# Kernel tuning notes

Measured on AMD Instinct MI355X. Metric: run time of the kernel, lower is better.

## Reference

```python
import jax, jax.numpy as jnp
import numpy as np

ALPHA = 0.2  # LeakyReLU negative slope
NEG_BIG = -9e15


def setup_inputs() -> dict:
    key = jax.random.key(0)
    k1, k2, k3, k4 = jax.random.split(key, 4)
    B, N, Fin, Fout = 16, 1024, 256, 256
    h = jax.random.normal(k1, (B, N, Fin), dtype=jnp.float32)
    adj = jax.random.randint(k2, (B, N, N), 0, 2, dtype=jnp.int32)
    # xavier_uniform with gain=1.414
    def xavier(k, shape, gain=1.414):
        fan_in, fan_out = shape[0], shape[1]
        bound = gain * np.sqrt(6.0 / (fan_in + fan_out))
        return jax.random.uniform(k, shape, jnp.float32, -bound, bound)
    W = xavier(k3, (Fin, Fout))
    a = xavier(k4, (2 * Fout, 1))
    return {"h": h, "adj": adj, "W": W, "a": a}


def reference(h, adj, W, a):
    # h: [B,N,Fin], adj: [B,N,N], W: [Fin,Fout], a: [2*Fout,1]
    Fout = W.shape[1]
    Wh = jnp.einsum('bnf,fo->bno', h, W)                      # [B,N,Fout]
    a1, a2 = a[:Fout, 0], a[Fout:, 0]                          # [Fout], [Fout]
    # e_ij = leakyrelu(Wh_i . a1 + Wh_j . a2) -- outer sum, no O(N^2*F) tensor
    f1 = Wh @ a1                                               # [B,N]
    f2 = Wh @ a2                                               # [B,N]
    e = jax.nn.leaky_relu(f1[:, :, None] + f2[:, None, :], negative_slope=ALPHA)
    attention = jnp.where(adj > 0, e, jnp.float32(NEG_BIG))    # [B,N,N]
    attention = jax.nn.softmax(attention, axis=2)
    h_prime = jnp.einsum('bij,bjo->bio', attention, Wh)        # [B,N,Fout]
    return jax.nn.elu(h_prime)
```

## Files before the change

### kernel.cpp

```cpp
#include <hip/hip_runtime.h>
#include <hip/hip_bf16.h>

#define Bsz 16
#define Nn  1024
#define Ff  256
#define ALPHA 0.2f
#define NEG_BIG -9.0e15f

typedef __attribute__((ext_vector_type(8))) short short8;
typedef __attribute__((ext_vector_type(4))) float f32x4;
typedef __attribute__((ext_vector_type(4))) unsigned short ushort4_t;

__device__ __forceinline__ unsigned short f2bf(float x) {
    union { __hip_bfloat16 b; unsigned short u; } cv;
    cv.b = __float2bfloat16(x);
    return cv.u;
}

__global__ __launch_bounds__(256) void gat_prep(
    const float* __restrict__ W, const float* __restrict__ a,
    float* __restrict__ w1, float* __restrict__ w2)
{
    const int t = threadIdx.x, w = t >> 6, ln = t & 63;
    __shared__ float a1s[Ff], a2s[Ff];
    a1s[t] = a[t];
    a2s[t] = a[Ff + t];
    __syncthreads();
    const int f = blockIdx.x * 4 + w;
    float s1 = 0.f, s2 = 0.f;
    #pragma unroll
    for (int c = 0; c < 4; c++) {
        const int o = ln + 64 * c;
        const float wv = W[(size_t)f * Ff + o];
        s1 += wv * a1s[o];
        s2 += wv * a2s[o];
    }
    #pragma unroll
    for (int off = 1; off < 64; off <<= 1) {
        s1 += __shfl_xor(s1, off, 64);
        s2 += __shfl_xor(s2, off, 64);
    }
    if (ln == 0) { w1[f] = s1; w2[f] = s2; }
}

__global__ __launch_bounds__(256) void pack_f(
    const float* __restrict__ h, const float* __restrict__ W,
    const float* __restrict__ w1, const float* __restrict__ w2,
    unsigned short* __restrict__ hK, unsigned short* __restrict__ WK,
    float* __restrict__ f1, float* __restrict__ f2)
{
    __shared__ __align__(16) float tile[32][258];
    const int id = blockIdx.x, t = threadIdx.x, w = t >> 6, ln = t & 63;
    const bool isH = (id < 512);
    const float* src;
    unsigned short* dst;
    int grow0 = 0;
    if (isH) {
        const int b = id >> 5, kt = id & 31;
        grow0 = b * Nn + kt * 32;
        src = h + (size_t)grow0 * Ff;
        dst = hK + ((size_t)(b * 32 + kt)) * 8192;
    } else {
        const int ft = id - 512;
        src = W + (size_t)ft * 32 * Ff;
        dst = WK + (size_t)ft * 8192;
    }
    #pragma unroll
    for (int rr = 0; rr < 8; rr++) {
        const int row = rr * 4 + w;
        const int col = ln * 4;
        const float4 v = *(const float4*)&src[row * Ff + col];
        float2* tr = (float2*)&tile[row][col];
        tr[0] = make_float2(v.x, v.y);
        tr[1] = make_float2(v.z, v.w);
    }
    __syncthreads();

    unsigned* d32 = (unsigned*)dst;
    #pragma unroll
    for (int k = 0; k < 16; k++) {
        const int fidx = k * 256 + t;
        const int o = fidx >> 4, q = fidx & 15;
        const unsigned lo = f2bf(tile[2 * q][o]);
        const unsigned hi = f2bf(tile[2 * q + 1][o]);
        d32[fidx] = lo | (hi << 16);
    }

    if (isH) {
        float w1r[4], w2r[4];
        #pragma unroll
        for (int c = 0; c < 4; c++) {
            w1r[c] = w1[ln + 64 * c];
            w2r[c] = w2[ln + 64 * c];
        }
        #pragma unroll
        for (int rr = 0; rr < 8; rr++) {
            const int row = rr * 4 + w;
            float s1 = 0.f, s2 = 0.f;
            #pragma unroll
            for (int c = 0; c < 4; c++) {
                const float hv = tile[row][ln + 64 * c];
                s1 += hv * w1r[c];
                s2 += hv * w2r[c];
            }
            #pragma unroll
            for (int off = 1; off < 64; off <<= 1) {
                s1 += __shfl_xor(s1, off, 64);
                s2 += __shfl_xor(s2, off, 64);
            }
            if (ln == 0) { f1[grow0 + row] = s1; f2[grow0 + row] = s2; }
        }
    }
}

#define TI 32
__global__ __launch_bounds__(1024, 8) void gat_attn(
    const int* __restrict__ adj,
    const float* __restrict__ f1, const float* __restrict__ f2,
    const unsigned short* __restrict__ hK, const unsigned short* __restrict__ WK,
    float* __restrict__ out)
{
    __shared__ __align__(16) unsigned short pbf[TI * 1024];
    const int t = threadIdx.x, w = t >> 6, ln = t & 63;
    const int m = ln & 15, quad = ln >> 4;
    const int bid = blockIdx.x;
    const int b  = 2 * (bid & 7) + ((bid >> 3) & 1);
    const int i0 = (bid >> 4) * TI;

    const int r0 = 2 * w, r1 = r0 + 1;
    const int grb = b * Nn + i0 + r0;
    const int* aptr = adj + (size_t)grb * Nn;
    int4 av0[4], av1[4];
    #pragma unroll
    for (int c = 0; c < 4; c++) {
        av0[c] = *(const int4*)&aptr[c * 256 + 4 * ln];
        av1[c] = *(const int4*)&aptr[Nn + c * 256 + 4 * ln];
    }
    float4 f2r[4];
    #pragma unroll
    for (int c = 0; c < 4; c++)
        f2r[c] = *(const float4*)&f2[b * Nn + 256 * c + 4 * ln];

    const float fi0 = f1[grb], fi1 = f1[grb + 1];
    float e0[16], e1[16];
    float mx0 = -INFINITY, mx1 = -INFINITY;
    #pragma unroll
    for (int c = 0; c < 4; c++) {
        const float4 fv = f2r[c];
        float x, y;
        x = fi0 + fv.x; x = fmaxf(x, ALPHA * x); x = av0[c].x > 0 ? x : NEG_BIG; e0[4*c+0] = x;
        y = fi0 + fv.y; y = fmaxf(y, ALPHA * y); y = av0[c].y > 0 ? y : NEG_BIG; e0[4*c+1] = y;
        mx0 = fmaxf(fmaxf(x, y), mx0);
        x = fi0 + fv.z; x = fmaxf(x, ALPHA * x); x = av0[c].z > 0 ? x : NEG_BIG; e0[4*c+2] = x;
        y = fi0 + fv.w; y = fmaxf(y, ALPHA * y); y = av0[c].w > 0 ? y : NEG_BIG; e0[4*c+3] = y;
        mx0 = fmaxf(fmaxf(x, y), mx0);
        x = fi1 + fv.x; x = fmaxf(x, ALPHA * x); x = av1[c].x > 0 ? x : NEG_BIG; e1[4*c+0] = x;
        y = fi1 + fv.y; y = fmaxf(y, ALPHA * y); y = av1[c].y > 0 ? y : NEG_BIG; e1[4*c+1] = y;
        mx1 = fmaxf(fmaxf(x, y), mx1);
        x = fi1 + fv.z; x = fmaxf(x, ALPHA * x); x = av1[c].z > 0 ? x : NEG_BIG; e1[4*c+2] = x;
        y = fi1 + fv.w; y = fmaxf(y, ALPHA * y); y = av1[c].w > 0 ? y : NEG_BIG; e1[4*c+3] = y;
        mx1 = fmaxf(fmaxf(x, y), mx1);
    }
    #pragma unroll
    for (int off = 1; off < 64; off <<= 1) {
        mx0 = fmaxf(mx0, __shfl_xor(mx0, off, 64));
        mx1 = fmaxf(mx1, __shfl_xor(mx1, off, 64));
    }
    float s0 = 0.f, s1 = 0.f;
    #pragma unroll
    for (int c = 0; c < 16; c++) {
        e0[c] = __expf(e0[c] - mx0); s0 += e0[c];
        e1[c] = __expf(e1[c] - mx1); s1 += e1[c];
    }
    #pragma unroll
    for (int off = 1; off < 64; off <<= 1) {
        s0 += __shfl_xor(s0, off, 64);
        s1 += __shfl_xor(s1, off, 64);
    }
    const float ri0 = 1.f / s0, ri1 = 1.f / s1;
    const int sw0 = (r0 & 7) << 3, sw1 = (r1 & 7) << 3;
    #pragma unroll
    for (int c = 0; c < 4; c++) {
        const int j = 256 * c + 4 * ln;
        ushort4_t v0 = { f2bf(e0[4*c] * ri0), f2bf(e0[4*c+1] * ri0),
                         f2bf(e0[4*c+2] * ri0), f2bf(e0[4*c+3] * ri0) };
        ushort4_t v1 = { f2bf(e1[4*c] * ri1), f2bf(e1[4*c+1] * ri1),
                         f2bf(e1[4*c+2] * ri1), f2bf(e1[4*c+3] * ri1) };
        *(ushort4_t*)&pbf[r0 * 1024 + (j ^ sw0)] = v0;
        *(ushort4_t*)&pbf[r1 * 1024 + (j ^ sw1)] = v1;
    }

    const int n0 = w * 16;
    const unsigned short* hKb = hK + (size_t)b * 32 * 8192;
    const int arow0 = m * 1024, arow1 = (16 + m) * 1024;
    const int asw = (m & 7) << 3;
    #define AF0(kt) (*(const short8*)&pbf[arow0 + ((((kt) * 32) + quad * 8) ^ asw)])
    #define AF1(kt) (*(const short8*)&pbf[arow1 + ((((kt) * 32) + quad * 8) ^ asw)])
    #define BF(kt)  (*(const short8*)&hKb[(size_t)(kt) * 8192 + (n0 + m) * 32 + quad * 8])

    short8 bq0 = BF(0), bq1 = BF(1), bq2 = BF(2), bq3 = BF(3);
    __syncthreads();

    f32x4 acc0 = {0.f, 0.f, 0.f, 0.f}, acc1 = acc0;
    short8 a0c = AF0(0), a1c = AF1(0);
    __builtin_amdgcn_s_setprio(1);
    #pragma unroll
    for (int kt = 0; kt < 32; kt++) {
        short8 bnew = bq0, a0n = a0c, a1n = a1c;
        if (kt + 4 < 32) bnew = BF(kt + 4);
        if (kt + 1 < 32) { a0n = AF0(kt + 1); a1n = AF1(kt + 1); }
        acc0 = __builtin_amdgcn_mfma_f32_16x16x32_bf16(a0c, bq0, acc0, 0, 0, 0);
        acc1 = __builtin_amdgcn_mfma_f32_16x16x32_bf16(a1c, bq0, acc1, 0, 0, 0);
        a0c = a0n; a1c = a1n;
        bq0 = bq1; bq1 = bq2; bq2 = bq3; bq3 = bnew;
    }
    __builtin_amdgcn_s_setprio(0);

    #define WB(kt)  (*(const short8*)&WK[(size_t)(kt) * 8192 + (n0 + m) * 32 + quad * 8])
    short8 wbc = WB(0), wbn = WB(1);

    __syncthreads();
    #pragma unroll
    for (int reg = 0; reg < 4; reg++) {
        pbf[(quad * 4 + reg) * 264 + n0 + m]      = f2bf(acc0[reg]);
        pbf[(16 + quad * 4 + reg) * 264 + n0 + m] = f2bf(acc1[reg]);
    }
    __syncthreads();

    #define GA0(kt) (*(const short8*)&pbf[m * 264 + (kt) * 32 + quad * 8])
    #define GA1(kt) (*(const short8*)&pbf[(16 + m) * 264 + (kt) * 32 + quad * 8])

    f32x4 c0 = {0.f, 0.f, 0.f, 0.f}, c1 = c0;
    short8 ga0 = GA0(0), ga1 = GA1(0);
    __builtin_amdgcn_s_setprio(1);
    #pragma unroll
    for (int kt = 0; kt < 8; kt++) {
        short8 ga0n = ga0, ga1n = ga1, wnew = wbc;
        if (kt + 2 < 8) wnew = WB(kt + 2);
        if (kt + 1 < 8) { ga0n = GA0(kt + 1); ga1n = GA1(kt + 1); }
        c0 = __builtin_amdgcn_mfma_f32_16x16x32_bf16(ga0, wbc, c0, 0, 0, 0);
        c1 = __builtin_amdgcn_mfma_f32_16x16x32_bf16(ga1, wbc, c1, 0, 0, 0);
        ga0 = ga0n; ga1 = ga1n; wbc = wbn; wbn = wnew;
    }
    __builtin_amdgcn_s_setprio(0);
    const size_t ob = (size_t)(b * Nn) + i0;
    #pragma unroll
    for (int reg = 0; reg < 4; reg++) {
        float v;
        v = c0[reg]; v = v > 0.f ? v : (__expf(v) - 1.f);
        out[(ob + quad * 4 + reg) * Ff + n0 + m] = v;
        v = c1[reg]; v = v > 0.f ? v : (__expf(v) - 1.f);
        out[(ob + 16 + quad * 4 + reg) * Ff + n0 + m] = v;
    }
}

extern "C" void kernel_launch(void* const* d_in, const int* in_sizes, int n_in,
                              void* d_out, int out_size, void* d_ws, size_t ws_size,
                              hipStream_t stream)
{
    const void* h   = d_in[0];
    const void* adj = d_in[1];
    const void* W   = d_in[2];
    const void* a   = d_in[3];
    for (int i = 0; i < n_in; i++) {
        if      (in_sizes[i] == Bsz * Nn * Ff) h   = d_in[i];
        else if (in_sizes[i] == Bsz * Nn * Nn) adj = d_in[i];
        else if (in_sizes[i] == Ff * Ff)       W   = d_in[i];
        else if (in_sizes[i] == 2 * Ff)        a   = d_in[i];
    }
    float* out = (float*)d_out;

    char*  wsb = (char*)d_ws;
    float* w1  = (float*)wsb;
    float* w2  = w1 + Ff;
    float* f1  = (float*)(wsb + 4096);
    float* f2  = f1 + Bsz * Nn;
    unsigned short* hK = (unsigned short*)(wsb + 4096 + 2 * 65536);
    unsigned short* WK = hK + (size_t)Bsz * 32 * 8192;

    gat_prep<<<64, 256, 0, stream>>>((const float*)W, (const float*)a, w1, w2);
    pack_f<<<520, 256, 0, stream>>>((const float*)h, (const float*)W, w1, w2, hK, WK, f1, f2);
    gat_attn<<<Bsz * (Nn / TI), 1024, 0, stream>>>((const int*)adj, f1, f2, hK, WK, out);
}
```

Before: 138.7 us.

## Precompute Wh=hW in pack kernel and drop second GEMM from attention kernel

Reassociates (P·h)·W into P·(h·W): the pack kernel now multiplies h by W with MFMA and stores bf16 Wh tiles, and the WK bf16 packing moves into the prep kernel. The attention kernel then needs only one GEMM, removing the per-tile W GEMM, its LDS staging and two barriers. It adds an extra bf16 rounding of Wh and more work in the pack stage, and pads the LDS row stride.

```diff
diff --git a/kernel.cpp b/kernel.cpp
--- a/kernel.cpp
+++ b/kernel.cpp
@@ -19,52 +19,35 @@
 
 __global__ __launch_bounds__(256) void gat_prep(
     const float* __restrict__ W, const float* __restrict__ a,
-    float* __restrict__ w1, float* __restrict__ w2)
+    float* __restrict__ w1, float* __restrict__ w2,
+    unsigned short* __restrict__ WK)
 {
     const int t = threadIdx.x, w = t >> 6, ln = t & 63;
-    __shared__ float a1s[Ff], a2s[Ff];
-    a1s[t] = a[t];
-    a2s[t] = a[Ff + t];
-    __syncthreads();
-    const int f = blockIdx.x * 4 + w;
-    float s1 = 0.f, s2 = 0.f;
-    #pragma unroll
-    for (int c = 0; c < 4; c++) {
-        const int o = ln + 64 * c;
-        const float wv = W[(size_t)f * Ff + o];
-        s1 += wv * a1s[o];
-        s2 += wv * a2s[o];
-    }
-    #pragma unroll
-    for (int off = 1; off < 64; off <<= 1) {
-        s1 += __shfl_xor(s1, off, 64);
-        s2 += __shfl_xor(s2, off, 64);
-    }
-    if (ln == 0) { w1[f] = s1; w2[f] = s2; }
-}
-
-__global__ __launch_bounds__(256) void pack_f(
-    const float* __restrict__ h, const float* __restrict__ W,
-    const float* __restrict__ w1, const float* __restrict__ w2,
-    unsigned short* __restrict__ hK, unsigned short* __restrict__ WK,
-    float* __restrict__ f1, float* __restrict__ f2)
-{
+    if (blockIdx.x < 64) {
+        __shared__ float a1s[Ff], a2s[Ff];
+        a1s[t] = a[t];
+        a2s[t] = a[Ff + t];
+        __syncthreads();
+        const int f = blockIdx.x * 4 + w;
+        float s1 = 0.f, s2 = 0.f;
+        #pragma unroll
+        for (int c = 0; c < 4; c++) {
+            const int o = ln + 64 * c;
+            const float wv = W[(size_t)f * Ff + o];
+            s1 += wv * a1s[o];
+            s2 += wv * a2s[o];
+        }
+        #pragma unroll
+        for (int off = 1; off < 64; off <<= 1) {
+            s1 += __shfl_xor(s1, off, 64);
+            s2 += __shfl_xor(s2, off, 64);
+        }
+        if (ln == 0) { w1[f] = s1; w2[f] = s2; }
+        return;
+    }
     __shared__ __align__(16) float tile[32][258];
-    const int id = blockIdx.x, t = threadIdx.x, w = t >> 6, ln = t & 63;
-    const bool isH = (id < 512);
-    const float* src;
-    unsigned short* dst;
-    int grow0 = 0;
-    if (isH) {
-        const int b = id >> 5, kt = id & 31;
-        grow0 = b * Nn + kt * 32;
-        src = h + (size_t)grow0 * Ff;
-        dst = hK + ((size_t)(b * 32 + kt)) * 8192;
-    } else {
-        const int ft = id - 512;
-        src = W + (size_t)ft * 32 * Ff;
-        dst = WK + (size_t)ft * 8192;
-    }
+    const int ft = blockIdx.x - 64;
+    const float* src = W + (size_t)ft * 32 * Ff;
     #pragma unroll
     for (int rr = 0; rr < 8; rr++) {
         const int row = rr * 4 + w;
@@ -75,8 +58,7 @@
         tr[1] = make_float2(v.z, v.w);
     }
     __syncthreads();
-
-    unsigned* d32 = (unsigned*)dst;
+    unsigned* d32 = (unsigned*)(WK + (size_t)ft * 8192);
     #pragma unroll
     for (int k = 0; k < 16; k++) {
         const int fidx = k * 256 + t;
@@ -85,8 +67,30 @@
         const unsigned hi = f2bf(tile[2 * q + 1][o]);
         d32[fidx] = lo | (hi << 16);
     }
-
-    if (isH) {
+}
+
+__global__ __launch_bounds__(256) void pack_f(
+    const float* __restrict__ h, const unsigned short* __restrict__ WK,
+    const float* __restrict__ w1, const float* __restrict__ w2,
+    unsigned short* __restrict__ WhK,
+    float* __restrict__ f1, float* __restrict__ f2)
+{
+    __shared__ __align__(16) float tile[32][258];
+    const int id = blockIdx.x, t = threadIdx.x, w = t >> 6, ln = t & 63;
+    const int grow0 = id * 32;
+    const float* src = h + (size_t)grow0 * Ff;
+    #pragma unroll
+    for (int rr = 0; rr < 8; rr++) {
+        const int row = rr * 4 + w;
+        const int col = ln * 4;
+        const float4 v = *(const float4*)&src[row * Ff + col];
+        float2* tr = (float2*)&tile[row][col];
+        tr[0] = make_float2(v.x, v.y);
+        tr[1] = make_float2(v.z, v.w);
+    }
+    __syncthreads();
+
+    {
         float w1r[4], w2r[4];
         #pragma unroll
         for (int c = 0; c < 4; c++) {
@@ -111,16 +115,55 @@
             if (ln == 0) { f1[grow0 + row] = s1; f2[grow0 + row] = s2; }
         }
     }
+
+    const int m = ln & 15, quad = ln >> 4;
+    f32x4 acc0[4], acc1[4];
+    #pragma unroll
+    for (int nt = 0; nt < 4; nt++) {
+        f32x4 z = {0.f, 0.f, 0.f, 0.f};
+        acc0[nt] = z; acc1[nt] = z;
+    }
+    #pragma unroll
+    for (int kt = 0; kt < 8; kt++) {
+        short8 a0, a1;
+        {
+            const float* p0 = &tile[m][kt * 32 + quad * 8];
+            const float* p1 = &tile[16 + m][kt * 32 + quad * 8];
+            #pragma unroll
+            for (int e = 0; e < 8; e++) {
+                a0[e] = (short)f2bf(p0[e]);
+                a1[e] = (short)f2bf(p1[e]);
+            }
+        }
+        #pragma unroll
+        for (int nt = 0; nt < 4; nt++) {
+            const short8 bfr = *(const short8*)&WK[(size_t)kt * 8192 + (w * 64 + nt * 16 + m) * 32 + quad * 8];
+            acc0[nt] = __builtin_amdgcn_mfma_f32_16x16x32_bf16(a0, bfr, acc0[nt], 0, 0, 0);
+            acc1[nt] = __builtin_amdgcn_mfma_f32_16x16x32_bf16(a1, bfr, acc1[nt], 0, 0, 0);
+        }
+    }
+    unsigned short* dst = WhK + (size_t)id * 8192;
+    #pragma unroll
+    for (int nt = 0; nt < 4; nt++) {
+        const int o = w * 64 + nt * 16 + m;
+        ushort4_t v0 = { f2bf(acc0[nt][0]), f2bf(acc0[nt][1]),
+                         f2bf(acc0[nt][2]), f2bf(acc0[nt][3]) };
+        ushort4_t v1 = { f2bf(acc1[nt][0]), f2bf(acc1[nt][1]),
+                         f2bf(acc1[nt][2]), f2bf(acc1[nt][3]) };
+        *(ushort4_t*)&dst[o * 32 + quad * 4]      = v0;
+        *(ushort4_t*)&dst[o * 32 + 16 + quad * 4] = v1;
+    }
 }
 
 #define TI 32
+#define PST 1040
 __global__ __launch_bounds__(1024, 8) void gat_attn(
     const int* __restrict__ adj,
     const float* __restrict__ f1, const float* __restrict__ f2,
-    const unsigned short* __restrict__ hK, const unsigned short* __restrict__ WK,
+    const unsigned short* __restrict__ WhK,
     float* __restrict__ out)
 {
-    __shared__ __align__(16) unsigned short pbf[TI * 1024];
+    __shared__ __align__(16) unsigned short pbf[TI * PST];
     const int t = threadIdx.x, w = t >> 6, ln = t & 63;
     const int m = ln & 15, quad = ln >> 4;
     const int bid = blockIdx.x;
@@ -186,13 +229,13 @@
                          f2bf(e0[4*c+2] * ri0), f2bf(e0[4*c+3] * ri0) };
         ushort4_t v1 = { f2bf(e1[4*c] * ri1), f2bf(e1[4*c+1] * ri1),
                          f2bf(e1[4*c+2] * ri1), f2bf(e1[4*c+3] * ri1) };
-        *(ushort4_t*)&pbf[r0 * 1024 + (j ^ sw0)] = v0;
-        *(ushort4_t*)&pbf[r1 * 1024 + (j ^ sw1)] = v1;
+        *(ushort4_t*)&pbf[r0 * PST + (j ^ sw0)] = v0;
+        *(ushort4_t*)&pbf[r1 * PST + (j ^ sw1)] = v1;
     }
 
     const int n0 = w * 16;
-    const unsigned short* hKb = hK + (size_t)b * 32 * 8192;
-    const int arow0 = m * 1024, arow1 = (16 + m) * 1024;
+    const unsigned short* hKb = WhK + (size_t)b * 32 * 8192;
+    const int arow0 = m * PST, arow1 = (16 + m) * PST;
     const int asw = (m & 7) << 3;
     #define AF0(kt) (*(const short8*)&pbf[arow0 + ((((kt) * 32) + quad * 8) ^ asw)])
     #define AF1(kt) (*(const short8*)&pbf[arow1 + ((((kt) * 32) + quad * 8) ^ asw)])
@@ -216,40 +259,13 @@
     }
     __builtin_amdgcn_s_setprio(0);
 
-    #define WB(kt)  (*(const short8*)&WK[(size_t)(kt) * 8192 + (n0 + m) * 32 + quad * 8])
-    short8 wbc = WB(0), wbn = WB(1);
-
-    __syncthreads();
-    #pragma unroll
-    for (int reg = 0; reg < 4; reg++) {
-        pbf[(quad * 4 + reg) * 264 + n0 + m]      = f2bf(acc0[reg]);
-        pbf[(16 + quad * 4 + reg) * 264 + n0 + m] = f2bf(acc1[reg]);
-    }
-    __syncthreads();
-
-    #define GA0(kt) (*(const short8*)&pbf[m * 264 + (kt) * 32 + quad * 8])
-    #define GA1(kt) (*(const short8*)&pbf[(16 + m) * 264 + (kt) * 32 + quad * 8])
-
-    f32x4 c0 = {0.f, 0.f, 0.f, 0.f}, c1 = c0;
-    short8 ga0 = GA0(0), ga1 = GA1(0);
-    __builtin_amdgcn_s_setprio(1);
-    #pragma unroll
-    for (int kt = 0; kt < 8; kt++) {
-        short8 ga0n = ga0, ga1n = ga1, wnew = wbc;
-        if (kt + 2 < 8) wnew = WB(kt + 2);
-        if (kt + 1 < 8) { ga0n = GA0(kt + 1); ga1n = GA1(kt + 1); }
-        c0 = __builtin_amdgcn_mfma_f32_16x16x32_bf16(ga0, wbc, c0, 0, 0, 0);
-        c1 = __builtin_amdgcn_mfma_f32_16x16x32_bf16(ga1, wbc, c1, 0, 0, 0);
-        ga0 = ga0n; ga1 = ga1n; wbc = wbn; wbn = wnew;
-    }
-    __builtin_amdgcn_s_setprio(0);
     const size_t ob = (size_t)(b * Nn) + i0;
     #pragma unroll
     for (int reg = 0; reg < 4; reg++) {
         float v;
-        v = c0[reg]; v = v > 0.f ? v : (__expf(v) - 1.f);
+        v = acc0[reg]; v = v > 0.f ? v : (__expf(v) - 1.f);
         out[(ob + quad * 4 + reg) * Ff + n0 + m] = v;
-        v = c1[reg]; v = v > 0.f ? v : (__expf(v) - 1.f);
+        v = acc1[reg]; v = v > 0.f ? v : (__expf(v) - 1.f);
         out[(ob + 16 + quad * 4 + reg) * Ff + n0 + m] = v;
     }
 }
@@ -275,10 +291,10 @@
     float* w2  = w1 + Ff;
     float* f1  = (float*)(wsb + 4096);
     float* f2  = f1 + Bsz * Nn;
-    unsigned short* hK = (unsigned short*)(wsb + 4096 + 2 * 65536);
-    unsigned short* WK = hK + (size_t)Bsz * 32 * 8192;
-
-    gat_prep<<<64, 256, 0, stream>>>((const float*)W, (const float*)a, w1, w2);
-    pack_f<<<520, 256, 0, stream>>>((const float*)h, (const float*)W, w1, w2, hK, WK, f1, f2);
-    gat_attn<<<Bsz * (Nn / TI), 1024, 0, stream>>>((const int*)adj, f1, f2, hK, WK, out);
-}
+    unsigned short* WhK = (unsigned short*)(wsb + 4096 + 2 * 65536);
+    unsigned short* WK  = WhK + (size_t)Bsz * 32 * 8192;
+
+    gat_prep<<<72, 256, 0, stream>>>((const float*)W, (const float*)a, w1, w2, WK);
+    pack_f<<<512, 256, 0, stream>>>((const float*)h, WK, w1, w2, WhK, f1, f2);
+    gat_attn<<<Bsz * (Nn / TI), 1024, 0, stream>>>((const int*)adj, f1, f2, WhK, out);
+}
```

New measurement: 139.8 us. No clear change (+0.8%).
